# Optimization experiments

Measured on AMD Instinct MI355X. Metric: run time of the kernel, lower is better.

## Reference

```python
import jax, jax.numpy as jnp
import numpy as np

D_MODEL = 256
D_INNER = 512   # expand * d_model
NHEADS = 8
HEADDIM = 64    # d_inner // nheads
NGROUPS = 1
MDIST = 16


def setup_inputs() -> dict:
    key = jax.random.key(0)
    ks = jax.random.split(key, 12)
    B, L, Q = 4, 2048, 300
    in_key = jax.random.normal(ks[0], (B, L, D_MODEL), jnp.float32)
    in_query = jax.random.normal(ks[1], (B, Q, D_MODEL), jnp.float32)
    dist = jax.random.normal(ks[2], (B, L, Q, MDIST), jnp.float32)

    def lin(k, out_f, in_f):  # torch nn.Linear default init (kaiming-uniform-ish)
        bound = 1.0 / np.sqrt(in_f)
        return jax.random.uniform(k, (out_f, in_f), jnp.float32, -bound, bound)

    W_key = lin(ks[3], 2 * D_INNER + 2 * NGROUPS + NHEADS, D_MODEL)
    W_query = lin(ks[4], D_INNER, D_MODEL)
    W_bc = lin(ks[5], 2 * NGROUPS, MDIST)
    W_dt = lin(ks[6], NHEADS, MDIST)
    # dt_bias init (inverse-softplus of dt sampled log-uniform in [1e-4, 0.1])
    dt_min, dt_max = 1e-4, 0.1
    dtv = jnp.exp(jax.random.uniform(ks[7], (NHEADS,)) * (np.log(dt_max) - np.log(dt_min)) + np.log(dt_min))
    dtv = jnp.clip(dtv, 1e-4, None)
    dt_bias = dtv + jnp.log(-jnp.expm1(-dtv))
    A_log = jnp.log(jax.random.uniform(ks[8], (NHEADS,), minval=1.0, maxval=16.0))
    Dp = jnp.ones((NHEADS,), jnp.float32)
    W_out_key = lin(ks[9], D_MODEL, D_INNER)
    W_out_query = lin(ks[10], D_MODEL, D_INNER)
    key_norm_w = jnp.ones((D_INNER,), jnp.float32)
    ln_w = jnp.ones((D_INNER,), jnp.float32)
    ln_b = jnp.zeros((D_INNER,), jnp.float32)
    return dict(in_key=in_key, in_query=in_query, dist=dist, W_key=W_key, W_query=W_query,
                W_bc=W_bc, W_dt=W_dt, dt_bias=dt_bias, A_log=A_log, Dp=Dp,
                W_out_key=W_out_key, W_out_query=W_out_query, key_norm_w=key_norm_w,
                ln_w=ln_w, ln_b=ln_b)


def _issm_scan(x, S0, dt, A, Bm, Cm, Dp):
    """Selective scan with per-(l,h,n) dt and per-(l,n) B,C (ngroups=1).
    x: (B,L,H,P)  dt: (B,L,H,N)  Bm,Cm: (B,L,N)  S0: (B,H,P,N)  A: (H,)  Dp: (H,)
    """
    xs = (jnp.moveaxis(x, 1, 0), jnp.moveaxis(dt, 1, 0),
          jnp.moveaxis(Bm, 1, 0), jnp.moveaxis(Cm, 1, 0))

    def step(S, inp):
        xl, dtl, Bl, Cl = inp               # (B,H,P), (B,H,N), (B,N), (B,N)
        dA = jnp.exp(dtl * A[None, :, None])            # (B,H,N)
        dBx = (dtl * Bl[:, None, :])[:, :, None, :] * xl[:, :, :, None]
        S = S * dA[:, :, None, :] + dBx                 # (B,H,P,N)
        y = jnp.einsum('bhpn,bn->bhp', S, Cl) + Dp[None, :, None] * xl
        return S, y

    Sf, ys = jax.lax.scan(step, S0, xs)
    return jnp.moveaxis(ys, 0, 1), Sf       # (B,L,H,P), (B,H,P,N)


def reference(in_key, in_query, dist, W_key, W_query, W_bc, W_dt, dt_bias, A_log, Dp,
              W_out_key, W_out_query, key_norm_w, ln_w, ln_b):
    B, L, _ = in_key.shape
    Q = in_query.shape[1]
    zxbcdt = in_key @ W_key.T                            # (B,L,2*Din+2g+H)
    z = zxbcdt[..., :D_INNER]
    x = zxbcdt[..., D_INNER:2 * D_INNER].reshape(B, L, NHEADS, HEADDIM)
    b_bias = zxbcdt[..., 2 * D_INNER:2 * D_INNER + 1]    # (B,L,1)
    c_bias = zxbcdt[..., 2 * D_INNER + 1:2 * D_INNER + 2]
    dt_proj_bias = zxbcdt[..., 2 * D_INNER + 2:]         # (B,L,H)

    # initial state: (B,H,P,Q) -- state dim N == num_queries
    S0 = (in_query @ W_query.T).reshape(B, Q, NHEADS, HEADDIM).transpose(0, 2, 3, 1)
    A = -jnp.exp(A_log)                                  # (H,), constant over state dim

    bc = jnp.einsum('blqm,cm->blqc', dist, W_bc)         # (B,L,Q,2)
    Bm = bc[..., 0] + b_bias                             # (B,L,Q)
    Cm = bc[..., 1] + c_bias
    dtb = jnp.einsum('blqm,hm->blhq', dist, W_dt)        # (B,L,H,Q)
    dt = jax.nn.softplus(dtb + dt_proj_bias[..., None] + dt_bias[None, None, :, None])

    y_f, S_f = _issm_scan(x, S0, dt, A, Bm, Cm, Dp)
    # bidirectional: backward branch uses identical (cloned) x/B/C, flipped along L
    y_b, S_b = _issm_scan(x[:, ::-1], S0, dt[:, ::-1], A, Bm[:, ::-1], Cm[:, ::-1], Dp)
    y = (y_f + y_b[:, ::-1]) * 0.5
    S = (S_f + S_b) * 0.5

    key = y.reshape(B, L, D_INNER)
    g = key * jax.nn.silu(z)                             # gated RMSNorm, norm_before_gate=False
    key = g * jax.lax.rsqrt(jnp.mean(g * g, -1, keepdims=True) + 1e-5) * key_norm_w
    out_key = key @ W_out_key.T

    ls = S.transpose(0, 3, 1, 2).reshape(B, Q, D_INNER)  # b h p q -> b q (h p)
    mu = jnp.mean(ls, -1, keepdims=True)
    var = jnp.mean((ls - mu) ** 2, -1, keepdims=True)
    ls = (ls - mu) * jax.lax.rsqrt(var + 1e-5) * ln_w + ln_b
    out_query = ls @ W_out_query.T
    return out_key, out_query
```

## Files before the change

### kernel.cpp

```cpp
#include <hip/hip_runtime.h>
#include <hip/hip_bf16.h>

#define D_MODEL 256
#define D_INNER 512
#define NHEADS 8
#define HEADDIM 64
#define MDIST 16
#define BB 4
#define LL 2048
#define QQ 300
#define QP 320
#define NSEG 16
#define SEGLEN 128

typedef unsigned short ushort_t;
typedef __attribute__((ext_vector_type(8))) short bf16x8;
typedef __attribute__((ext_vector_type(4))) float f32x4;

__global__ __launch_bounds__(256) void c_split(const float* __restrict__ in,
                                               ushort_t* __restrict__ hi,
                                               ushort_t* __restrict__ lo, int n) {
    int i = blockIdx.x * 256 + threadIdx.x;
    if (i >= n) return;
    float v = in[i];
    __hip_bfloat16 h = __float2bfloat16(v);
    float hf = __bfloat162float(h);
    __hip_bfloat16 l = __float2bfloat16(v - hf);
    hi[i] = *(ushort_t*)&h;
    lo[i] = *(ushort_t*)&l;
}

__global__ __launch_bounds__(256) void gemm_bf16s(const ushort_t* __restrict__ Ah,
                                                  const ushort_t* __restrict__ Al,
                                                  const ushort_t* __restrict__ Bh,
                                                  const ushort_t* __restrict__ Bl,
                                                  float* __restrict__ C,
                                                  int M, int N, int K) {
    int w = threadIdx.x >> 6, lane = threadIdx.x & 63;
    int n0 = blockIdx.x * 64;
    int m0 = blockIdx.y * 128 + w * 32;
    int lm = lane & 15, lk = (lane >> 4) * 8;
    f32x4 acc[2][4];
#pragma unroll
    for (int i = 0; i < 2; i++)
#pragma unroll
        for (int j = 0; j < 4; j++) acc[i][j] = {0.f, 0.f, 0.f, 0.f};

    for (int k0 = 0; k0 < K; k0 += 32) {
        bf16x8 ah[2], al[2], bh[4], blo[4];
#pragma unroll
        for (int mf = 0; mf < 2; mf++) {
            int row = m0 + mf * 16 + lm;
            if (row >= M) row = M - 1;
            size_t off = (size_t)row * K + k0 + lk;
            ah[mf] = *(const bf16x8*)(Ah + off);
            al[mf] = *(const bf16x8*)(Al + off);
        }
#pragma unroll
        for (int nf = 0; nf < 4; nf++) {
            int col = n0 + nf * 16 + lm;
            size_t off = (size_t)col * K + k0 + lk;
            bh[nf]  = *(const bf16x8*)(Bh + off);
            blo[nf] = *(const bf16x8*)(Bl + off);
        }
#pragma unroll
        for (int mf = 0; mf < 2; mf++)
#pragma unroll
            for (int nf = 0; nf < 4; nf++) {
                acc[mf][nf] = __builtin_amdgcn_mfma_f32_16x16x32_bf16(ah[mf], bh[nf],  acc[mf][nf], 0, 0, 0);
                acc[mf][nf] = __builtin_amdgcn_mfma_f32_16x16x32_bf16(ah[mf], blo[nf], acc[mf][nf], 0, 0, 0);
                acc[mf][nf] = __builtin_amdgcn_mfma_f32_16x16x32_bf16(al[mf], bh[nf],  acc[mf][nf], 0, 0, 0);
            }
    }
#pragma unroll
    for (int mf = 0; mf < 2; mf++)
#pragma unroll
        for (int nf = 0; nf < 4; nf++)
#pragma unroll
            for (int r = 0; r < 4; r++) {
                int m = m0 + mf * 16 + (lane >> 4) * 4 + r;
                if (m < M) C[(size_t)m * N + n0 + nf * 16 + lm] = acc[mf][nf][r];
            }
}

__global__ __launch_bounds__(256) void k1b_bias(const float* __restrict__ in_key,
                                                const float* __restrict__ W_key,
                                                float* __restrict__ bias10) {
    int w = threadIdx.x >> 6, lane = threadIdx.x & 63;
    int row = blockIdx.x * 4 + w;
    float4 a = *(const float4*)(in_key + (size_t)row * 256 + lane * 4);
#pragma unroll
    for (int c = 0; c < 10; c++) {
        float4 b = *(const float4*)(W_key + (size_t)(1024 + c) * 256 + lane * 4);
        float t = a.x * b.x + a.y * b.y + a.z * b.z + a.w * b.w;
#pragma unroll
        for (int o = 32; o > 0; o >>= 1) t += __shfl_down(t, o, 64);
        if (lane == 0) bias10[row * 10 + c] = t;
    }
}

__global__ __launch_bounds__(256) void k2_dist(const float* __restrict__ dist,
                                               const float* __restrict__ bias10,
                                               const float* __restrict__ W_bc,
                                               const float* __restrict__ W_dt,
                                               const float* __restrict__ dt_bias,
                                               const float* __restrict__ A_log,
                                               float* __restrict__ dA,
                                               float* __restrict__ dtB,
                                               float* __restrict__ Cm) {
    __shared__ float sWbc[32], sWdt[128], sb[8], sA[8];
    int tid = threadIdx.x;
    if (tid < 32) sWbc[tid] = W_bc[tid];
    else if (tid < 160) sWdt[tid - 32] = W_dt[tid - 32];
    else if (tid < 168) sb[tid - 160] = dt_bias[tid - 160];
    else if (tid < 176) sA[tid - 168] = -expf(A_log[tid - 168]);
    __syncthreads();
    int gid = blockIdx.x * 256 + tid;
    if (gid >= BB * LL * QQ) return;
    int q = gid % QQ;
    int bl = gid / QQ;
    const float* dp = dist + (size_t)gid * 16;
    float d[16];
    float4 d0 = *(const float4*)(dp + 0);
    float4 d1 = *(const float4*)(dp + 4);
    float4 d2 = *(const float4*)(dp + 8);
    float4 d3 = *(const float4*)(dp + 12);
    d[0]=d0.x; d[1]=d0.y; d[2]=d0.z; d[3]=d0.w;
    d[4]=d1.x; d[5]=d1.y; d[6]=d1.z; d[7]=d1.w;
    d[8]=d2.x; d[9]=d2.y; d[10]=d2.z; d[11]=d2.w;
    d[12]=d3.x; d[13]=d3.y; d[14]=d3.z; d[15]=d3.w;
    float bc0 = 0.f, bc1 = 0.f;
#pragma unroll
    for (int m = 0; m < 16; m++) {
        bc0 = fmaf(d[m], sWbc[m], bc0);
        bc1 = fmaf(d[m], sWbc[16 + m], bc1);
    }
    float Bmv = bc0 + bias10[bl * 10 + 0];
    float Cv  = bc1 + bias10[bl * 10 + 1];
    Cm[bl * QP + q] = Cv;
#pragma unroll
    for (int h = 0; h < 8; h++) {
        float t = 0.f;
#pragma unroll
        for (int m = 0; m < 16; m++) t = fmaf(d[m], sWdt[h * 16 + m], t);
        float pre = t + bias10[bl * 10 + 2 + h] + sb[h];
        float dt = (pre > 20.f) ? pre : log1pf(expf(pre));
        int o = (bl * 8 + h) * QP + q;
        dA[o]  = expf(sA[h] * dt);
        dtB[o] = dt * Bmv;
    }
}

__global__ __launch_bounds__(256) void k2b_segdecay(const float* __restrict__ dA,
                                                    float* __restrict__ segd) {
    int gid = blockIdx.x * 256 + threadIdx.x;
    if (gid >= BB * NSEG * 8 * QP) return;
    int q = gid % QP; int r = gid / QP;
    int h = r % 8; r /= 8;
    int s = r % NSEG; int b = r / NSEG;
    int base = ((b * LL + s * SEGLEN) * 8 + h) * QP + q;
    float p = 1.f;
    for (int i = 0; i < SEGLEN; i++) p *= dA[base + i * 8 * QP];
    segd[gid] = p;
}

__global__ __launch_bounds__(512) void pass_a(const float* __restrict__ dA,
                                              const float* __restrict__ dtB,
                                              const float* __restrict__ zx,
                                              float* __restrict__ S_local) {
    __shared__ __align__(16) float sOp[2][4][704];
    int seg = blockIdx.x, bh = blockIdx.y, dir = blockIdx.z;
    int tid = threadIdx.x;
    int w = tid >> 6, lane = tid & 63;
    int nn = lane & 7, pp = lane >> 3;
    int p = w * 8 + pp;
    int b = bh >> 3, h = bh & 7;
    float S[40];
#pragma unroll
    for (int j = 0; j < 40; j++) S[j] = 0.f;

    auto stage = [&](int g, int buf) {
#pragma unroll
        for (int k = 0; k < 2; k++) {
            int idx = tid + k * 512;
            if (idx < 704) {
                int it = idx / 176;
                int pos = (idx % 176) * 4;
                int i = g * 4 + it;
                int l = dir ? (LL - 1 - (seg * SEGLEN + i)) : (seg * SEGLEN + i);
                int bl = b * LL + l;
                const float* src;
                if (pos < 320)      src = dA  + (size_t)(bl * 8 + h) * QP + pos;
                else if (pos < 640) src = dtB + (size_t)(bl * 8 + h) * QP + (pos - 320);
                else                src = zx + (size_t)bl * 1024 + 512 + h * 64 + (pos - 640);
                *(float4*)&sOp[buf][it][pos] = *(const float4*)src;
            }
        }
    };
    stage(0, 0);
    for (int g = 0; g < SEGLEN / 4; g++) {
        __syncthreads();
        if (g + 1 < SEGLEN / 4) stage(g + 1, (g + 1) & 1);
#pragma unroll
        for (int it = 0; it < 4; it++) {
            const float* bufc = sOp[g & 1][it];
            float x = bufc[640 + p];
#pragma unroll
            for (int c = 0; c < 10; c++) {
                float4 a4 = *(const float4*)(bufc + nn * 40 + c * 4);
                float4 b4 = *(const float4*)(bufc + 320 + nn * 40 + c * 4);
                S[c * 4 + 0] = fmaf(S[c * 4 + 0], a4.x, b4.x * x);
                S[c * 4 + 1] = fmaf(S[c * 4 + 1], a4.y, b4.y * x);
                S[c * 4 + 2] = fmaf(S[c * 4 + 2], a4.z, b4.z * x);
                S[c * 4 + 3] = fmaf(S[c * 4 + 3], a4.w, b4.w * x);
            }
        }
    }
    size_t base = (size_t)((dir * NSEG + seg) * 32 + bh) * QP * 64;
#pragma unroll
    for (int j = 0; j < 40; j++)
        S_local[base + (size_t)(nn * 40 + j) * 64 + p] = S[j];
}

__global__ __launch_bounds__(256) void pass_b(const float* __restrict__ S_local,
                                              const float* __restrict__ segd,
                                              const float* __restrict__ S0q,
                                              float* __restrict__ S_in,
                                              float* __restrict__ Savg) {
    int gid = blockIdx.x * 256 + threadIdx.x;
    if (gid >= BB * 8 * QP * 64) return;
    int p = gid & 63; int r = gid >> 6;
    int n = r % QP; r /= QP;
    int h = r & 7; int b = r >> 3;
    int bh = b * 8 + h;
    float s0 = (n < QQ) ? S0q[(size_t)(b * QQ + n) * 512 + h * 64 + p] : 0.f;
    float Sf = 0.f, Sb = 0.f;
    for (int dir = 0; dir < 2; dir++) {
        float S = s0;
        for (int s = 0; s < NSEG; s++) {
            size_t idx = (size_t)(((dir * NSEG + s) * 32 + bh) * QP + n) * 64 + p;
            S_in[idx] = S;
            int sf = dir ? (NSEG - 1 - s) : s;
            float dec = segd[((b * NSEG + sf) * 8 + h) * QP + n];
            S = fmaf(S, dec, S_local[idx]);
        }
        if (dir == 0) Sf = S; else Sb = S;
    }
    Savg[((bh) * QP + n) * 64 + p] = 0.5f * (Sf + Sb);
}

__global__ __launch_bounds__(512) void pass_c(const float* __restrict__ dA,
                                              const float* __restrict__ dtB,
                                              const float* __restrict__ Cm,
                                              const float* __restrict__ zx,
                                              const float* __restrict__ S_in,
                                              float* __restrict__ yf,
                                              float* __restrict__ yb) {
    __shared__ __align__(16) float sOp[2][4][1024];
    int seg = blockIdx.x, bh = blockIdx.y, dir = blockIdx.z;
    int tid = threadIdx.x;
    int w = tid >> 6, lane = tid & 63;
    int nn = lane & 7, pp = lane >> 3;
    int p = w * 8 + pp;
    int b = bh >> 3, h = bh & 7;
    float S[40];
    size_t sbase = (size_t)((dir * NSEG + seg) * 32 + bh) * QP * 64;
#pragma unroll
    for (int j = 0; j < 40; j++) S[j] = S_in[sbase + (size_t)(nn * 40 + j) * 64 + p];
    float* __restrict__ yo = dir ? yb : yf;

    auto stage = [&](int g, int buf) {
#pragma unroll
        for (int k = 0; k < 2; k++) {
            int idx = tid + k * 512;
            int it = idx >> 8;
            int pos = (idx & 255) * 4;
            int i = g * 4 + it;
            int l = dir ? (LL - 1 - (seg * SEGLEN + i)) : (seg * SEGLEN + i);
            int bl = b * LL + l;
            const float* src;
            if (pos < 320)      src = dA  + (size_t)(bl * 8 + h) * QP + pos;
            else if (pos < 640) src = dtB + (size_t)(bl * 8 + h) * QP + (pos - 320);
            else if (pos < 960) src = Cm + (size_t)bl * QP + (pos - 640);
            else                src = zx + (size_t)bl * 1024 + 512 + h * 64 + (pos - 960);
            *(float4*)&sOp[buf][it][pos] = *(const float4*)src;
        }
    };
    stage(0, 0);
    for (int g = 0; g < SEGLEN / 4; g++) {
        __syncthreads();
        if (g + 1 < SEGLEN / 4) stage(g + 1, (g + 1) & 1);
#pragma unroll
        for (int it = 0; it < 4; it++) {
            int i = g * 4 + it;
            int l = dir ? (LL - 1 - (seg * SEGLEN + i)) : (seg * SEGLEN + i);
            int bl = b * LL + l;
            const float* bufc = sOp[g & 1][it];
            float x = bufc[960 + p];
            float y = 0.f;
#pragma unroll
            for (int c = 0; c < 10; c++) {
                float4 a4 = *(const float4*)(bufc + nn * 40 + c * 4);
                float4 b4 = *(const float4*)(bufc + 320 + nn * 40 + c * 4);
                float4 c4 = *(const float4*)(bufc + 640 + nn * 40 + c * 4);
                S[c * 4 + 0] = fmaf(S[c * 4 + 0], a4.x, b4.x * x); y = fmaf(S[c * 4 + 0], c4.x, y);
                S[c * 4 + 1] = fmaf(S[c * 4 + 1], a4.y, b4.y * x); y = fmaf(S[c * 4 + 1], c4.y, y);
                S[c * 4 + 2] = fmaf(S[c * 4 + 2], a4.z, b4.z * x); y = fmaf(S[c * 4 + 2], c4.z, y);
                S[c * 4 + 3] = fmaf(S[c * 4 + 3], a4.w, b4.w * x); y = fmaf(S[c * 4 + 3], c4.w, y);
            }
            y += __shfl_xor(y, 1, 64);
            y += __shfl_xor(y, 2, 64);
            y += __shfl_xor(y, 4, 64);
            if (nn == 0) yo[(size_t)(bl * 8 + h) * 64 + p] = y;
        }
    }
}

__global__ __launch_bounds__(512) void k4_gate(const float* __restrict__ yf,
                                               const float* __restrict__ yb,
                                               const float* __restrict__ zx,
                                               const float* __restrict__ Dp,
                                               const float* __restrict__ knw,
                                               float* __restrict__ key) {
    int bl = blockIdx.x;
    int t = threadIdx.x;
    int h = t >> 6;
    float x = zx[(size_t)bl * 1024 + 512 + t];
    float yv = 0.5f * (yf[(size_t)bl * 512 + t] + yb[(size_t)bl * 512 + t]) + Dp[h] * x;
    float z = zx[(size_t)bl * 1024 + t];
    float g = yv * (z / (1.f + expf(-z)));
    float v = g * g;
#pragma unroll
    for (int o = 32; o > 0; o >>= 1) v += __shfl_down(v, o, 64);
    __shared__ float rs[8];
    __shared__ float stot;
    if ((t & 63) == 0) rs[t >> 6] = v;
    __syncthreads();
    if (t == 0) {
        float s = 0.f;
#pragma unroll
        for (int i = 0; i < 8; i++) s += rs[i];
        stot = s;
    }
    __syncthreads();
    float rms = rsqrtf(stot / 512.f + 1e-5f);
    key[(size_t)bl * 512 + t] = g * rms * knw[t];
}

__global__ __launch_bounds__(512) void k5_ln(const float* __restrict__ Savg,
                                             const float* __restrict__ lnw,
                                             const float* __restrict__ lnb,
                                             float* __restrict__ lsn) {
    int bq = blockIdx.x;
    int b = bq / QQ, q = bq % QQ;
    int t = threadIdx.x;
    int h = t >> 6, p = t & 63;
    float v = Savg[((b * 8 + h) * QP + q) * 64 + p];
    float s1 = v, s2 = v * v;
#pragma unroll
    for (int o = 32; o > 0; o >>= 1) {
        s1 += __shfl_down(s1, o, 64);
        s2 += __shfl_down(s2, o, 64);
    }
    __shared__ float r1[8], r2[8];
    __shared__ float smu, srv;
    if ((t & 63) == 0) { r1[t >> 6] = s1; r2[t >> 6] = s2; }
    __syncthreads();
    if (t == 0) {
        float a = 0.f, c = 0.f;
#pragma unroll
        for (int i = 0; i < 8; i++) { a += r1[i]; c += r2[i]; }
        float mu = a / 512.f;
        float var = c / 512.f - mu * mu;
        smu = mu;
        srv = rsqrtf(var + 1e-5f);
    }
    __syncthreads();
    lsn[(size_t)bq * 512 + t] = (v - smu) * srv * lnw[t] + lnb[t];
}

extern "C" void kernel_launch(void* const* d_in, const int* in_sizes, int n_in,
                              void* d_out, int out_size, void* d_ws, size_t ws_size,
                              hipStream_t stream) {
    const float* in_key    = (const float*)d_in[0];
    const float* in_query  = (const float*)d_in[1];
    const float* dist      = (const float*)d_in[2];
    const float* W_key     = (const float*)d_in[3];
    const float* W_query   = (const float*)d_in[4];
    const float* W_bc      = (const float*)d_in[5];
    const float* W_dt      = (const float*)d_in[6];
    const float* dt_bias   = (const float*)d_in[7];
    const float* A_log     = (const float*)d_in[8];
    const float* Dp        = (const float*)d_in[9];
    const float* W_out_key = (const float*)d_in[10];
    const float* W_out_query = (const float*)d_in[11];
    const float* key_norm_w = (const float*)d_in[12];
    const float* ln_w      = (const float*)d_in[13];
    const float* ln_b      = (const float*)d_in[14];

    float* out_key = (float*)d_out;
    float* out_query = out_key + (size_t)BB * LL * D_MODEL;

    char* w8 = (char*)d_ws;
    auto alloc = [&](size_t bytes) {
        char* ptr = w8;
        w8 += (bytes + 255) & ~(size_t)255;
        return ptr;
    };
    float* zx     = (float*)alloc((size_t)8192 * 1024 * 4);
    float* bias10 = (float*)alloc((size_t)8192 * 10 * 4);
    float* S0q    = (float*)alloc((size_t)1200 * 512 * 4);
    float* dAb    = (float*)alloc((size_t)8192 * 8 * QP * 4);
    float* dtBb   = (float*)alloc((size_t)8192 * 8 * QP * 4);
    float* Cmb    = (float*)alloc((size_t)8192 * QP * 4);
    float* segd   = (float*)alloc((size_t)BB * NSEG * 8 * QP * 4);
    float* Sloc   = (float*)alloc((size_t)2 * NSEG * 32 * QP * 64 * 4);
    float* Sin    = (float*)alloc((size_t)2 * NSEG * 32 * QP * 64 * 4);
    float* yfb    = (float*)alloc((size_t)8192 * 512 * 4);
    float* ybb    = (float*)alloc((size_t)8192 * 512 * 4);
    float* Savg   = (float*)alloc((size_t)32 * QP * 64 * 4);
    float* keyb   = (float*)alloc((size_t)8192 * 512 * 4);
    float* lsn    = (float*)alloc((size_t)1200 * 512 * 4);
    ushort_t* ink_h  = (ushort_t*)alloc((size_t)2097152 * 2);
    ushort_t* ink_l  = (ushort_t*)alloc((size_t)2097152 * 2);
    ushort_t* wk_h   = (ushort_t*)alloc((size_t)262144 * 2);
    ushort_t* wk_l   = (ushort_t*)alloc((size_t)262144 * 2);
    ushort_t* inq_h  = (ushort_t*)alloc((size_t)307200 * 2);
    ushort_t* inq_l  = (ushort_t*)alloc((size_t)307200 * 2);
    ushort_t* wq_h   = (ushort_t*)alloc((size_t)131072 * 2);
    ushort_t* wq_l   = (ushort_t*)alloc((size_t)131072 * 2);
    ushort_t* keyb_h = (ushort_t*)alloc((size_t)4194304 * 2);
    ushort_t* keyb_l = (ushort_t*)alloc((size_t)4194304 * 2);
    ushort_t* wok_h  = (ushort_t*)alloc((size_t)131072 * 2);
    ushort_t* wok_l  = (ushort_t*)alloc((size_t)131072 * 2);
    ushort_t* lsn_h  = (ushort_t*)alloc((size_t)614400 * 2);
    ushort_t* lsn_l  = (ushort_t*)alloc((size_t)614400 * 2);
    ushort_t* woq_h  = (ushort_t*)alloc((size_t)131072 * 2);
    ushort_t* woq_l  = (ushort_t*)alloc((size_t)131072 * 2);

    c_split<<<8192, 256, 0, stream>>>(in_key, ink_h, ink_l, 2097152);
    c_split<<<1024, 256, 0, stream>>>(W_key, wk_h, wk_l, 262144);
    c_split<<<1200, 256, 0, stream>>>(in_query, inq_h, inq_l, 307200);
    c_split<<<512, 256, 0, stream>>>(W_query, wq_h, wq_l, 131072);
    c_split<<<512, 256, 0, stream>>>(W_out_key, wok_h, wok_l, 131072);
    c_split<<<512, 256, 0, stream>>>(W_out_query, woq_h, woq_l, 131072);

    gemm_bf16s<<<dim3(16, 64), 256, 0, stream>>>(ink_h, ink_l, wk_h, wk_l, zx, 8192, 1024, 256);
    k1b_bias<<<2048, 256, 0, stream>>>(in_key, W_key, bias10);
    gemm_bf16s<<<dim3(8, 10), 256, 0, stream>>>(inq_h, inq_l, wq_h, wq_l, S0q, 1200, 512, 256);

    k2_dist<<<9600, 256, 0, stream>>>(dist, bias10, W_bc, W_dt, dt_bias, A_log, dAb, dtBb, Cmb);
    k2b_segdecay<<<640, 256, 0, stream>>>(dAb, segd);

    pass_a<<<dim3(NSEG, 32, 2), 512, 0, stream>>>(dAb, dtBb, zx, Sloc);
    pass_b<<<2560, 256, 0, stream>>>(Sloc, segd, S0q, Sin, Savg);
    pass_c<<<dim3(NSEG, 32, 2), 512, 0, stream>>>(dAb, dtBb, Cmb, zx, Sin, yfb, ybb);

    k4_gate<<<8192, 512, 0, stream>>>(yfb, ybb, zx, Dp, key_norm_w, keyb);
    c_split<<<16384, 256, 0, stream>>>(keyb, keyb_h, keyb_l, 4194304);
    gemm_bf16s<<<dim3(4, 64), 256, 0, stream>>>(keyb_h, keyb_l, wok_h, wok_l, out_key, 8192, 256, 512);

    k5_ln<<<1200, 512, 0, stream>>>(Savg, ln_w, ln_b, lsn);
    c_split<<<2400, 256, 0, stream>>>(lsn, lsn_h, lsn_l, 614400);
    gemm_bf16s<<<dim3(4, 10), 256, 0, stream>>>(lsn_h, lsn_l, woq_h, woq_l, out_query, 1200, 256, 512);
}
```

Measured before the change: 1.076 ms.

## Fuse intra-segment output into pass A and add inter-segment correction via MFMA

Pass A now computes the local (zero-initialised) chunk outputs y along with the local states, reducing across 8 waves through shared memory. The sequential second scan pass C is replaced by a correction kernel that adds C·cumprod(dA)·S_in as a matrix product using split-bf16 MFMA. This removes a full recurrent rescan of each segment in exchange for a tensor-core GEMM with prefix products of decay. The new partitioning has each wave own 40 states for all 64 p, and the correction relies on the 3-term bf16 split to retain fp32-like accuracy.

Result: faster. 896.3 us (-16.7%).

```diff
diff --git a/kernel.cpp b/kernel.cpp
--- a/kernel.cpp
+++ b/kernel.cpp
@@ -17,17 +17,23 @@
 typedef __attribute__((ext_vector_type(8))) short bf16x8;
 typedef __attribute__((ext_vector_type(4))) float f32x4;
 
+__device__ __forceinline__ void bf16_split(float v, ushort_t& hi, ushort_t& lo) {
+    __hip_bfloat16 h = __float2bfloat16(v);
+    float hf = __bfloat162float(h);
+    __hip_bfloat16 l = __float2bfloat16(v - hf);
+    hi = *(ushort_t*)&h;
+    lo = *(ushort_t*)&l;
+}
+
 __global__ __launch_bounds__(256) void c_split(const float* __restrict__ in,
                                                ushort_t* __restrict__ hi,
                                                ushort_t* __restrict__ lo, int n) {
     int i = blockIdx.x * 256 + threadIdx.x;
     if (i >= n) return;
-    float v = in[i];
-    __hip_bfloat16 h = __float2bfloat16(v);
-    float hf = __bfloat162float(h);
-    __hip_bfloat16 l = __float2bfloat16(v - hf);
-    hi[i] = *(ushort_t*)&h;
-    lo[i] = *(ushort_t*)&l;
+    ushort_t h, l;
+    bf16_split(in[i], h, l);
+    hi[i] = h;
+    lo[i] = l;
 }
 
 __global__ __launch_bounds__(256) void gemm_bf16s(const ushort_t* __restrict__ Ah,
@@ -164,62 +170,91 @@
     segd[gid] = p;
 }
 
-__global__ __launch_bounds__(512) void pass_a(const float* __restrict__ dA,
-                                              const float* __restrict__ dtB,
-                                              const float* __restrict__ zx,
-                                              float* __restrict__ S_local) {
-    __shared__ __align__(16) float sOp[2][4][704];
+__global__ __launch_bounds__(512) void pass_ac(const float* __restrict__ dA,
+                                               const float* __restrict__ dtB,
+                                               const float* __restrict__ Cm,
+                                               const float* __restrict__ zx,
+                                               float* __restrict__ S_local,
+                                               float* __restrict__ yf,
+                                               float* __restrict__ yb) {
+    __shared__ __align__(16) float sOp[2][4][1024];
+    __shared__ float ybuf[2][4][8][64];
     int seg = blockIdx.x, bh = blockIdx.y, dir = blockIdx.z;
     int tid = threadIdx.x;
     int w = tid >> 6, lane = tid & 63;
-    int nn = lane & 7, pp = lane >> 3;
-    int p = w * 8 + pp;
+    int n0 = w * 40;
     int b = bh >> 3, h = bh & 7;
     float S[40];
 #pragma unroll
     for (int j = 0; j < 40; j++) S[j] = 0.f;
+    float* __restrict__ yo = dir ? yb : yf;
 
     auto stage = [&](int g, int buf) {
 #pragma unroll
         for (int k = 0; k < 2; k++) {
             int idx = tid + k * 512;
-            if (idx < 704) {
-                int it = idx / 176;
-                int pos = (idx % 176) * 4;
-                int i = g * 4 + it;
-                int l = dir ? (LL - 1 - (seg * SEGLEN + i)) : (seg * SEGLEN + i);
-                int bl = b * LL + l;
-                const float* src;
-                if (pos < 320)      src = dA  + (size_t)(bl * 8 + h) * QP + pos;
-                else if (pos < 640) src = dtB + (size_t)(bl * 8 + h) * QP + (pos - 320);
-                else                src = zx + (size_t)bl * 1024 + 512 + h * 64 + (pos - 640);
-                *(float4*)&sOp[buf][it][pos] = *(const float4*)src;
-            }
+            int it = idx >> 8;
+            int pos = (idx & 255) * 4;
+            int i = g * 4 + it;
+            int l = dir ? (LL - 1 - (seg * SEGLEN + i)) : (seg * SEGLEN + i);
+            int bl = b * LL + l;
+            const float* src;
+            if (pos < 320)      src = dA  + (size_t)(bl * 8 + h) * QP + pos;
+            else if (pos < 640) src = dtB + (size_t)(bl * 8 + h) * QP + (pos - 320);
+            else if (pos < 960) src = Cm + (size_t)bl * QP + (pos - 640);
+            else                src = zx + (size_t)bl * 1024 + 512 + h * 64 + (pos - 960);
+            *(float4*)&sOp[buf][it][pos] = *(const float4*)src;
         }
     };
     stage(0, 0);
     for (int g = 0; g < SEGLEN / 4; g++) {
         __syncthreads();
         if (g + 1 < SEGLEN / 4) stage(g + 1, (g + 1) & 1);
+        if (g > 0 && tid < 256) {
+            int it = tid >> 6, p = tid & 63;
+            int i = (g - 1) * 4 + it;
+            int l = dir ? (LL - 1 - (seg * SEGLEN + i)) : (seg * SEGLEN + i);
+            int bl = b * LL + l;
+            const float* yb0 = &ybuf[(g - 1) & 1][it][0][p];
+            float t = 0.f;
+#pragma unroll
+            for (int ww = 0; ww < 8; ww++) t += yb0[ww * 64];
+            yo[(size_t)(bl * 8 + h) * 64 + p] = t;
+        }
 #pragma unroll
         for (int it = 0; it < 4; it++) {
             const float* bufc = sOp[g & 1][it];
-            float x = bufc[640 + p];
+            float x = bufc[960 + lane];
+            float y = 0.f;
 #pragma unroll
             for (int c = 0; c < 10; c++) {
-                float4 a4 = *(const float4*)(bufc + nn * 40 + c * 4);
-                float4 b4 = *(const float4*)(bufc + 320 + nn * 40 + c * 4);
-                S[c * 4 + 0] = fmaf(S[c * 4 + 0], a4.x, b4.x * x);
-                S[c * 4 + 1] = fmaf(S[c * 4 + 1], a4.y, b4.y * x);
-                S[c * 4 + 2] = fmaf(S[c * 4 + 2], a4.z, b4.z * x);
-                S[c * 4 + 3] = fmaf(S[c * 4 + 3], a4.w, b4.w * x);
+                float4 a4 = *(const float4*)(bufc + n0 + c * 4);
+                float4 b4 = *(const float4*)(bufc + 320 + n0 + c * 4);
+                float4 c4 = *(const float4*)(bufc + 640 + n0 + c * 4);
+                S[c * 4 + 0] = fmaf(S[c * 4 + 0], a4.x, b4.x * x); y = fmaf(S[c * 4 + 0], c4.x, y);
+                S[c * 4 + 1] = fmaf(S[c * 4 + 1], a4.y, b4.y * x); y = fmaf(S[c * 4 + 1], c4.y, y);
+                S[c * 4 + 2] = fmaf(S[c * 4 + 2], a4.z, b4.z * x); y = fmaf(S[c * 4 + 2], c4.z, y);
+                S[c * 4 + 3] = fmaf(S[c * 4 + 3], a4.w, b4.w * x); y = fmaf(S[c * 4 + 3], c4.w, y);
             }
-        }
+            ybuf[g & 1][it][w][lane] = y;
+        }
+    }
+    __syncthreads();
+    if (tid < 256) {
+        int it = tid >> 6, p = tid & 63;
+        int i = (SEGLEN / 4 - 1) * 4 + it;
+        int l = dir ? (LL - 1 - (seg * SEGLEN + i)) : (seg * SEGLEN + i);
+        int bl = b * LL + l;
+        const float* yb0 = &ybuf[1][it][0][p];
+        float t = 0.f;
+#pragma unroll
+        for (int ww = 0; ww < 8; ww++) t += yb0[ww * 64];
+        yo[(size_t)(bl * 8 + h) * 64 + p] = t;
     }
     size_t base = (size_t)((dir * NSEG + seg) * 32 + bh) * QP * 64;
 #pragma unroll
     for (int j = 0; j < 40; j++)
-        S_local[base + (size_t)(nn * 40 + j) * 64 + p] = S[j];
+        S_local[base + (size_t)(n0 + j) * 64 + lane] = S[j];
 }
 
 __global__ __launch_bounds__(256) void pass_b(const float* __restrict__ S_local,
@@ -249,71 +284,110 @@
     Savg[((bh) * QP + n) * 64 + p] = 0.5f * (Sf + Sb);
 }
 
-__global__ __launch_bounds__(512) void pass_c(const float* __restrict__ dA,
-                                              const float* __restrict__ dtB,
-                                              const float* __restrict__ Cm,
-                                              const float* __restrict__ zx,
-                                              const float* __restrict__ S_in,
-                                              float* __restrict__ yf,
-                                              float* __restrict__ yb) {
-    __shared__ __align__(16) float sOp[2][4][1024];
+__global__ __launch_bounds__(256) void k3_corr(const float* __restrict__ dA,
+                                               const float* __restrict__ Cm,
+                                               const float* __restrict__ Sin,
+                                               float* __restrict__ yf,
+                                               float* __restrict__ yb) {
+    __shared__ __align__(16) ushort_t sAh[128][48], sAl[128][48];
+    __shared__ __align__(16) ushort_t sBh[64][48], sBl[64][48];
+    __shared__ float pref[8][32];
     int seg = blockIdx.x, bh = blockIdx.y, dir = blockIdx.z;
+    int b = bh >> 3, h = bh & 7;
     int tid = threadIdx.x;
     int w = tid >> 6, lane = tid & 63;
-    int nn = lane & 7, pp = lane >> 3;
-    int p = w * 8 + pp;
-    int b = bh >> 3, h = bh & 7;
-    float S[40];
-    size_t sbase = (size_t)((dir * NSEG + seg) * 32 + bh) * QP * 64;
-#pragma unroll
-    for (int j = 0; j < 40; j++) S[j] = S_in[sbase + (size_t)(nn * 40 + j) * 64 + p];
-    float* __restrict__ yo = dir ? yb : yf;
-
-    auto stage = [&](int g, int buf) {
-#pragma unroll
-        for (int k = 0; k < 2; k++) {
-            int idx = tid + k * 512;
-            int it = idx >> 8;
-            int pos = (idx & 255) * 4;
-            int i = g * 4 + it;
+    int lm = lane & 15, lkq = lane >> 4;
+    f32x4 acc[2][4];
+#pragma unroll
+    for (int i = 0; i < 2; i++)
+#pragma unroll
+        for (int j = 0; j < 4; j++) acc[i][j] = {0.f, 0.f, 0.f, 0.f};
+    size_t sinBase = (size_t)((dir * NSEG + seg) * 32 + bh) * QP * 64;
+    int nl = tid & 31, iseg = tid >> 5;
+
+    for (int k0 = 0; k0 < QP; k0 += 32) {
+        __syncthreads();
+#pragma unroll
+        for (int r = 0; r < 8; r++) {
+            int flat = tid + r * 256;
+            int kn = flat >> 6, p = flat & 63;
+            float v = Sin[sinBase + (size_t)(k0 + kn) * 64 + p];
+            ushort_t hi, lo;
+            bf16_split(v, hi, lo);
+            sBh[p][kn] = hi;
+            sBl[p][kn] = lo;
+        }
+        float da[16], cm[16];
+#pragma unroll
+        for (int k = 0; k < 16; k++) {
+            int i = iseg * 16 + k;
             int l = dir ? (LL - 1 - (seg * SEGLEN + i)) : (seg * SEGLEN + i);
             int bl = b * LL + l;
-            const float* src;
-            if (pos < 320)      src = dA  + (size_t)(bl * 8 + h) * QP + pos;
-            else if (pos < 640) src = dtB + (size_t)(bl * 8 + h) * QP + (pos - 320);
-            else if (pos < 960) src = Cm + (size_t)bl * QP + (pos - 640);
-            else                src = zx + (size_t)bl * 1024 + 512 + h * 64 + (pos - 960);
-            *(float4*)&sOp[buf][it][pos] = *(const float4*)src;
-        }
-    };
-    stage(0, 0);
-    for (int g = 0; g < SEGLEN / 4; g++) {
+            da[k] = dA[(size_t)(bl * 8 + h) * QP + k0 + nl];
+            cm[k] = Cm[(size_t)bl * QP + k0 + nl];
+        }
+        float lp = 1.f;
+#pragma unroll
+        for (int k = 0; k < 16; k++) lp *= da[k];
+        pref[iseg][nl] = lp;
         __syncthreads();
-        if (g + 1 < SEGLEN / 4) stage(g + 1, (g + 1) & 1);
-#pragma unroll
-        for (int it = 0; it < 4; it++) {
-            int i = g * 4 + it;
-            int l = dir ? (LL - 1 - (seg * SEGLEN + i)) : (seg * SEGLEN + i);
-            int bl = b * LL + l;
-            const float* bufc = sOp[g & 1][it];
-            float x = bufc[960 + p];
-            float y = 0.f;
-#pragma unroll
-            for (int c = 0; c < 10; c++) {
-                float4 a4 = *(const float4*)(bufc + nn * 40 + c * 4);
-                float4 b4 = *(const float4*)(bufc + 320 + nn * 40 + c * 4);
-                float4 c4 = *(const float4*)(bufc + 640 + nn * 40 + c * 4);
-                S[c * 4 + 0] = fmaf(S[c * 4 + 0], a4.x, b4.x * x); y = fmaf(S[c * 4 + 0], c4.x, y);
-                S[c * 4 + 1] = fmaf(S[c * 4 + 1], a4.y, b4.y * x); y = fmaf(S[c * 4 + 1], c4.y, y);
-                S[c * 4 + 2] = fmaf(S[c * 4 + 2], a4.z, b4.z * x); y = fmaf(S[c * 4 + 2], c4.z, y);
-                S[c * 4 + 3] = fmaf(S[c * 4 + 3], a4.w, b4.w * x); y = fmaf(S[c * 4 + 3], c4.w, y);
+        if (tid < 32) {
+            float c = 1.f;
+#pragma unroll
+            for (int s = 0; s < 8; s++) {
+                float t = pref[s][tid];
+                pref[s][tid] = c;
+                c *= t;
             }
-            y += __shfl_xor(y, 1, 64);
-            y += __shfl_xor(y, 2, 64);
-            y += __shfl_xor(y, 4, 64);
-            if (nn == 0) yo[(size_t)(bl * 8 + h) * 64 + p] = y;
-        }
-    }
+        }
+        __syncthreads();
+        float cum = pref[iseg][nl];
+#pragma unroll
+        for (int k = 0; k < 16; k++) {
+            cum *= da[k];
+            float v = cum * cm[k];
+            ushort_t hi, lo;
+            bf16_split(v, hi, lo);
+            int i = iseg * 16 + k;
+            sAh[i][nl] = hi;
+            sAl[i][nl] = lo;
+        }
+        __syncthreads();
+        bf16x8 ah[2], al[2], bhf[4], blf[4];
+#pragma unroll
+        for (int mf = 0; mf < 2; mf++) {
+            int row = w * 32 + mf * 16 + lm;
+            ah[mf] = *(const bf16x8*)&sAh[row][lkq * 8];
+            al[mf] = *(const bf16x8*)&sAl[row][lkq * 8];
+        }
+#pragma unroll
+        for (int nf = 0; nf < 4; nf++) {
+            int p = nf * 16 + lm;
+            bhf[nf] = *(const bf16x8*)&sBh[p][lkq * 8];
+            blf[nf] = *(const bf16x8*)&sBl[p][lkq * 8];
+        }
+#pragma unroll
+        for (int mf = 0; mf < 2; mf++)
+#pragma unroll
+            for (int nf = 0; nf < 4; nf++) {
+                acc[mf][nf] = __builtin_amdgcn_mfma_f32_16x16x32_bf16(ah[mf], bhf[nf], acc[mf][nf], 0, 0, 0);
+                acc[mf][nf] = __builtin_amdgcn_mfma_f32_16x16x32_bf16(ah[mf], blf[nf], acc[mf][nf], 0, 0, 0);
+                acc[mf][nf] = __builtin_amdgcn_mfma_f32_16x16x32_bf16(al[mf], bhf[nf], acc[mf][nf], 0, 0, 0);
+            }
+    }
+    float* __restrict__ yo = dir ? yb : yf;
+#pragma unroll
+    for (int mf = 0; mf < 2; mf++)
+#pragma unroll
+        for (int nf = 0; nf < 4; nf++)
+#pragma unroll
+            for (int r = 0; r < 4; r++) {
+                int i = w * 32 + mf * 16 + lkq * 4 + r;
+                int p = nf * 16 + lm;
+                int l = dir ? (LL - 1 - (seg * SEGLEN + i)) : (seg * SEGLEN + i);
+                size_t idx = (size_t)((b * LL + l) * 8 + h) * 64 + p;
+                yo[idx] += acc[mf][nf][r];
+            }
 }
 
 __global__ __launch_bounds__(512) void k4_gate(const float* __restrict__ yf,
@@ -452,9 +526,9 @@
     k2_dist<<<9600, 256, 0, stream>>>(dist, bias10, W_bc, W_dt, dt_bias, A_log, dAb, dtBb, Cmb);
     k2b_segdecay<<<640, 256, 0, stream>>>(dAb, segd);
 
-    pass_a<<<dim3(NSEG, 32, 2), 512, 0, stream>>>(dAb, dtBb, zx, Sloc);
+    pass_ac<<<dim3(NSEG, 32, 2), 512, 0, stream>>>(dAb, dtBb, Cmb, zx, Sloc, yfb, ybb);
     pass_b<<<2560, 256, 0, stream>>>(Sloc, segd, S0q, Sin, Savg);
-    pass_c<<<dim3(NSEG, 32, 2), 512, 0, stream>>>(dAb, dtBb, Cmb, zx, Sin, yfb, ybb);
+    k3_corr<<<dim3(NSEG, 32, 2), 256, 0, stream>>>(dAb, Cmb, Sin, yfb, ybb);
 
     k4_gate<<<8192, 512, 0, stream>>>(yfb, ybb, zx, Dp, key_norm_w, keyb);
     c_split<<<16384, 256, 0, stream>>>(keyb, keyb_h, keyb_l, 4194304);
```
